# Optimization experiments

Hardware: AMD Instinct MI355X
Metric: run time of the kernel (lower is better)

The kernel has to match this reference:

```python
import jax, jax.numpy as jnp
import numpy as np

B, S, D, H = 2, 2048, 1024, 16
DH = D // H
DFF = 4 * D
EPS = 1e-5


def layer_norm(x, w, b):
    m = jnp.mean(x, axis=-1, keepdims=True)
    v = jnp.mean((x - m) ** 2, axis=-1, keepdims=True)
    return (x - m) / jnp.sqrt(v + EPS) * w + b


def setup_inputs() -> dict:
    key = jax.random.key(0)
    ks = jax.random.split(key, 12)
    s = 0.02
    x = jax.random.normal(ks[0], (B, S, D), dtype=jnp.float32)
    mask = jnp.tril(jnp.ones((S, S), dtype=jnp.int32))  # causal mask, 0 = blocked
    Wq = jax.random.normal(ks[1], (H, D, DH), dtype=jnp.float32) * s
    Wk = jax.random.normal(ks[2], (H, D, DH), dtype=jnp.float32) * s
    Wv = jax.random.normal(ks[3], (H, D, DH), dtype=jnp.float32) * s
    Wo = jax.random.normal(ks[4], (D, D), dtype=jnp.float32) * s
    bo = jnp.zeros((D,), dtype=jnp.float32)
    W1 = jax.random.normal(ks[5], (D, DFF), dtype=jnp.float32) * s
    b1 = jnp.zeros((DFF,), dtype=jnp.float32)
    W2 = jax.random.normal(ks[6], (DFF, D), dtype=jnp.float32) * s
    b2 = jnp.zeros((D,), dtype=jnp.float32)
    ln1_w = jnp.ones((D,), dtype=jnp.float32)
    ln1_b = jnp.zeros((D,), dtype=jnp.float32)
    ln2_w = jnp.ones((D,), dtype=jnp.float32)
    ln2_b = jnp.zeros((D,), dtype=jnp.float32)
    return {"x": x, "mask": mask, "Wq": Wq, "Wk": Wk, "Wv": Wv, "Wo": Wo,
            "bo": bo, "W1": W1, "b1": b1, "W2": W2, "b2": b2,
            "ln1_w": ln1_w, "ln1_b": ln1_b, "ln2_w": ln2_w, "ln2_b": ln2_b}


def reference(x, mask, Wq, Wk, Wv, Wo, bo, W1, b1, W2, b2,
              ln1_w, ln1_b, ln2_w, ln2_b):
    # --- pre-LN attention ---
    xn = layer_norm(x, ln1_w, ln1_b)
    q = jnp.einsum('bsd,hdk->bhsk', xn, Wq)  # [B,H,S,DH]
    k = jnp.einsum('bsd,hdk->bhsk', xn, Wk)
    v = jnp.einsum('bsd,hdk->bhsk', xn, Wv)
    scores = jnp.einsum('bhik,bhjk->bhij', q, k) / jnp.sqrt(jnp.float32(DH))
    scores = jnp.where(mask == 0, jnp.float32(-1e9), scores)  # mask broadcasts [S,S]->[B,H,S,S]
    attn = jax.nn.softmax(scores, axis=-1)
    o = jnp.einsum('bhij,bhjk->bhik', attn, v)        # [B,H,S,DH]
    o = o.transpose(0, 2, 1, 3).reshape(x.shape[0], x.shape[1], D)  # concat heads
    attn_out = o @ Wo + bo
    x = x + attn_out
    # --- pre-LN FFN ---
    xn2 = layer_norm(x, ln2_w, ln2_b)
    h = jax.nn.relu(xn2 @ W1 + b1)
    x = x + (h @ W2 + b2)
    return x
```

## Files before the change

### kernel.cpp

```cpp
#include <hip/hip_runtime.h>
#include <hip/hip_bf16.h>
#include <stdint.h>

#define DEV static __device__ __forceinline__

using f32x4  = __attribute__((ext_vector_type(4))) float;
using bf16x4 = __attribute__((ext_vector_type(4))) __bf16;
using bf16x8 = __attribute__((ext_vector_type(8))) __bf16;

constexpr int SEQ = 2048;

DEV unsigned short f2bf(float f) {
  union { float f; unsigned u; } c; c.f = f;
  unsigned u = c.u;
  u += 0x7fffu + ((u >> 16) & 1u);
  return (unsigned short)(u >> 16);
}

DEV float wred_sum(float v) {
  #pragma unroll
  for (int m = 32; m > 0; m >>= 1) v += __shfl_xor(v, m, 64);
  return v;
}

DEV void g2l16(const unsigned short* g, unsigned short* l) {
  __builtin_amdgcn_global_load_lds(
      (const __attribute__((address_space(1))) void*)g,
      (__attribute__((address_space(3))) void*)l, 16, 0, 0);
}

DEV int xcd_map(int bid, int nwg) {
  const int cpx = nwg >> 3;
  return (bid & 7) * cpx + (bid >> 3);
}

__global__ __launch_bounds__(256) void convw_all(
    const float* __restrict__ Wq, const float* __restrict__ Wk,
    const float* __restrict__ Wv, const float* __restrict__ Wo,
    const float* __restrict__ W1, const float* __restrict__ W2,
    unsigned short* __restrict__ WqkvT, unsigned short* __restrict__ WoT,
    unsigned short* __restrict__ W1T,   unsigned short* __restrict__ W2T)
{
  const int blk = blockIdx.x;
  const float* inh; unsigned short* outh; int K, Nh, n0, k0;
  if (blk < 768) {
    const int seg = blk >> 8, l = blk & 255;
    const int head = l >> 4, kt = l & 15;
    const float* in = seg == 0 ? Wq : seg == 1 ? Wk : Wv;
    inh  = in + (size_t)head * 1024 * 64;
    outh = WqkvT + (size_t)seg * 1024 * 1024 + (size_t)head * 64 * 1024;
    K = 1024; Nh = 64; n0 = 0; k0 = kt * 64;
  } else if (blk < 1024) {
    const int l = blk - 768; inh = Wo; outh = WoT; K = 1024; Nh = 1024;
    n0 = (l & 15) * 64; k0 = (l >> 4) * 64;
  } else if (blk < 2048) {
    const int l = blk - 1024; inh = W1; outh = W1T; K = 1024; Nh = 4096;
    n0 = (l & 63) * 64; k0 = (l >> 6) * 64;
  } else {
    const int l = blk - 2048; inh = W2; outh = W2T; K = 4096; Nh = 1024;
    n0 = (l & 15) * 64; k0 = (l >> 4) * 64;
  }
  __shared__ float t[64][65];
  const int tid = threadIdx.x;
  #pragma unroll
  for (int r = 0; r < 4; ++r) {
    const int idx = tid + 256 * r;
    const int k = idx >> 4, c = (idx & 15) * 4;
    const float4 v = *(const float4*)(inh + (size_t)(k0 + k) * Nh + n0 + c);
    t[c + 0][k] = v.x; t[c + 1][k] = v.y; t[c + 2][k] = v.z; t[c + 3][k] = v.w;
  }
  __syncthreads();
  #pragma unroll
  for (int r = 0; r < 4; ++r) {
    const int idx = tid + 256 * r;
    const int n = idx >> 4, k4 = (idx & 15) * 4;
    ushort4 o;
    o.x = f2bf(t[n][k4 + 0]); o.y = f2bf(t[n][k4 + 1]);
    o.z = f2bf(t[n][k4 + 2]); o.w = f2bf(t[n][k4 + 3]);
    *(ushort4*)(outh + (size_t)(n0 + n) * K + k0 + k4) = o;
  }
}

__global__ __launch_bounds__(256) void ln_kernel(
    const float* __restrict__ x, const float* __restrict__ w,
    const float* __restrict__ b, unsigned short* __restrict__ out)
{
  const int row = blockIdx.x;
  const int tid = threadIdx.x;
  const float4 v = ((const float4*)(x + (size_t)row * 1024))[tid];
  float s  = v.x + v.y + v.z + v.w;
  float s2 = v.x*v.x + v.y*v.y + v.z*v.z + v.w*v.w;
  s = wred_sum(s); s2 = wred_sum(s2);
  __shared__ float rs[4], rs2[4];
  const int wave = tid >> 6, lane = tid & 63;
  if (lane == 0) { rs[wave] = s; rs2[wave] = s2; }
  __syncthreads();
  const float S  = rs[0] + rs[1] + rs[2] + rs[3];
  const float S2 = rs2[0] + rs2[1] + rs2[2] + rs2[3];
  const float mean = S * (1.f / 1024.f);
  const float var  = S2 * (1.f / 1024.f) - mean * mean;
  const float inv  = rsqrtf(var + 1e-5f);
  const float4 wv = ((const float4*)w)[tid];
  const float4 bv = ((const float4*)b)[tid];
  ushort4 o;
  o.x = f2bf((v.x - mean) * inv * wv.x + bv.x);
  o.y = f2bf((v.y - mean) * inv * wv.y + bv.y);
  o.z = f2bf((v.z - mean) * inv * wv.z + bv.z);
  o.w = f2bf((v.w - mean) * inv * wv.w + bv.w);
  ((ushort4*)(out + (size_t)row * 1024))[tid] = o;
}

template<int EPI>
__global__ __launch_bounds__(256) void gemm_kp(
    const unsigned short* __restrict__ A, const unsigned short* __restrict__ BT,
    void* __restrict__ Cout, const float* __restrict__ bias,
    const float* __restrict__ res, int M, int N, int K)
{
  __shared__ unsigned short sA[3][128 * 64];
  __shared__ unsigned short sB[3][64 * 64];
  const int tid = threadIdx.x;
  const int wave = tid >> 6, lane = tid & 63;
  const int wr = wave >> 1, wc = wave & 1;
  const int bid = xcd_map(blockIdx.y * gridDim.x + blockIdx.x, gridDim.x * gridDim.y);
  const int m0 = (bid / gridDim.x) * 128, n0 = (bid % gridDim.x) * 64;
  const int lr = lane & 15, lg = lane >> 4;
  const int wb = tid & 192;

  const f32x4 zero = {0.f, 0.f, 0.f, 0.f};
  f32x4 acc[4][2];
  #pragma unroll
  for (int i = 0; i < 4; ++i)
    #pragma unroll
    for (int j = 0; j < 2; ++j) acc[i][j] = zero;

  auto STAGE = [&](int slot, int kt) {
    const int k0 = kt * 64;
    #pragma unroll
    for (int r = 0; r < 4; ++r) {
      const int c = tid + 256 * r;
      const int row = c >> 3;
      const int so = ((c & 7) ^ (row & 7)) * 8;
      g2l16(A + (size_t)(m0 + row) * K + k0 + so, sA[slot] + (size_t)(wb + 256 * r) * 8);
    }
    #pragma unroll
    for (int r = 0; r < 2; ++r) {
      const int c = tid + 256 * r;
      const int row = c >> 3;
      const int so = ((c & 7) ^ (row & 7)) * 8;
      g2l16(BT + (size_t)(n0 + row) * K + k0 + so, sB[slot] + (size_t)(wb + 256 * r) * 8);
    }
  };

  const int nt = K / 64;
  STAGE(0, 0); STAGE(1, 1);

  for (int t = 0; t < nt; ++t) {
    asm volatile("s_waitcnt vmcnt(6)" ::: "memory");
    __builtin_amdgcn_s_barrier();
    const int slot = t % 3;
    bf16x8 af[4][2], bfr[2][2];
    #pragma unroll
    for (int i = 0; i < 4; ++i) {
      const int row = wr * 64 + i * 16 + lr;
      #pragma unroll
      for (int kk = 0; kk < 2; ++kk)
        af[i][kk] = *(const bf16x8*)(sA[slot] + row * 64 + (((kk * 4 + lg) ^ (row & 7)) << 3));
    }
    #pragma unroll
    for (int j = 0; j < 2; ++j) {
      const int row = wc * 32 + j * 16 + lr;
      #pragma unroll
      for (int kk = 0; kk < 2; ++kk)
        bfr[j][kk] = *(const bf16x8*)(sB[slot] + row * 64 + (((kk * 4 + lg) ^ (row & 7)) << 3));
    }
    __builtin_amdgcn_s_setprio(1);
    #pragma unroll
    for (int i = 0; i < 4; ++i)
      #pragma unroll
      for (int j = 0; j < 2; ++j)
        #pragma unroll
        for (int kk = 0; kk < 2; ++kk)
          acc[i][j] = __builtin_amdgcn_mfma_f32_16x16x32_bf16(af[i][kk], bfr[j][kk], acc[i][j], 0, 0, 0);
    __builtin_amdgcn_s_setprio(0);
    const int nx = (t + 2 < nt) ? t + 2 : nt - 1;
    STAGE((t + 2) % 3, nx);
  }
  asm volatile("s_waitcnt vmcnt(0)" ::: "memory");

  #pragma unroll
  for (int i = 0; i < 4; ++i) {
    #pragma unroll
    for (int j = 0; j < 2; ++j) {
      #pragma unroll
      for (int r = 0; r < 4; ++r) {
        const int row = m0 + wr * 64 + i * 16 + lg * 4 + r;
        const int col = n0 + wc * 32 + j * 16 + lr;
        const float v = acc[i][j][r];
        if (EPI == 1) {
          ((float*)Cout)[(size_t)row * N + col] = v + bias[col] + res[(size_t)row * N + col];
        } else {
          ((unsigned short*)Cout)[(size_t)row * N + col] = f2bf(v);
        }
      }
    }
  }
}

template<int EPI>
__global__ __launch_bounds__(512) void gemm256(
    const unsigned short* __restrict__ A, const unsigned short* __restrict__ BT,
    void* __restrict__ Cout, const float* __restrict__ bias,
    int M, int N, int K)
{
  __shared__ unsigned short sA[2][256 * 64];
  __shared__ unsigned short sB[2][256 * 64];
  const int tid = threadIdx.x;
  const int lane = tid & 63;
  const int wave = tid >> 6;
  const int wm = wave >> 2, wn = wave & 3;
  const int bid = xcd_map(blockIdx.y * gridDim.x + blockIdx.x, gridDim.x * gridDim.y);
  const int m0 = (bid / gridDim.x) * 256, n0 = (bid % gridDim.x) * 256;
  const int lr = lane & 15, lg = lane >> 4;

  const f32x4 zero = {0.f, 0.f, 0.f, 0.f};
  f32x4 acc[8][4];
  #pragma unroll
  for (int i = 0; i < 8; ++i)
    #pragma unroll
    for (int j = 0; j < 4; ++j) acc[i][j] = zero;

  auto STAGE = [&](int buf, int k0) {
    #pragma unroll
    for (int r = 0; r < 4; ++r) {
      const int c = tid + 512 * r;
      const int row = c >> 3;
      const int slot = (c & 7) ^ (row & 7);
      const int cb = (tid & 448) + 512 * r;
      g2l16(A  + (size_t)(m0 + row) * K + k0 + slot * 8, sA[buf] + (size_t)cb * 8);
      g2l16(BT + (size_t)(n0 + row) * K + k0 + slot * 8, sB[buf] + (size_t)cb * 8);
    }
  };
  auto RD = [&](const unsigned short* base, int R, int C) -> const bf16x8* {
    return (const bf16x8*)(base + R * 64 + ((((C >> 3) ^ (R & 7))) << 3));
  };

  const int nt = K / 64;
  STAGE(0, 0);
  asm volatile("s_waitcnt vmcnt(0)" ::: "memory");
  __syncthreads();

  for (int t = 0; t < nt; ++t) {
    const int buf = t & 1;
    if (t + 1 < nt) STAGE(buf ^ 1, (t + 1) * 64);
    #pragma unroll
    for (int p = 0; p < 4; ++p) {
      const int ih = p >> 1, jh = p & 1;
      bf16x8 af[4][2], bfr[2][2];
      #pragma unroll
      for (int i = 0; i < 4; ++i)
        #pragma unroll
        for (int kk = 0; kk < 2; ++kk)
          af[i][kk] = *RD(sA[buf], wm * 128 + (ih * 4 + i) * 16 + lr, kk * 32 + lg * 8);
      #pragma unroll
      for (int j = 0; j < 2; ++j)
        #pragma unroll
        for (int kk = 0; kk < 2; ++kk)
          bfr[j][kk] = *RD(sB[buf], wn * 64 + (jh * 2 + j) * 16 + lr, kk * 32 + lg * 8);
      __builtin_amdgcn_s_setprio(1);
      #pragma unroll
      for (int i = 0; i < 4; ++i)
        #pragma unroll
        for (int j = 0; j < 2; ++j)
          #pragma unroll
          for (int kk = 0; kk < 2; ++kk)
            acc[ih * 4 + i][jh * 2 + j] = __builtin_amdgcn_mfma_f32_16x16x32_bf16(
                af[i][kk], bfr[j][kk], acc[ih * 4 + i][jh * 2 + j], 0, 0, 0);
      __builtin_amdgcn_s_setprio(0);
      if (p < 3) __builtin_amdgcn_s_barrier();
    }
    asm volatile("s_waitcnt vmcnt(0)" ::: "memory");
    __builtin_amdgcn_s_barrier();
  }

  #pragma unroll
  for (int i = 0; i < 8; ++i) {
    #pragma unroll
    for (int j = 0; j < 4; ++j) {
      #pragma unroll
      for (int r = 0; r < 4; ++r) {
        const int row = m0 + wm * 128 + i * 16 + lg * 4 + r;
        const int col = n0 + wn * 64 + j * 16 + lr;
        float v = acc[i][j][r];
        if (EPI == 0) {
          if (col < 1024) v *= 0.18033688f;
          ((unsigned short*)Cout)[(size_t)row * N + col] = f2bf(v);
        } else {
          float t2 = v + bias[col];
          t2 = t2 > 0.f ? t2 : 0.f;
          ((unsigned short*)Cout)[(size_t)row * N + col] = f2bf(t2);
        }
      }
    }
  }
}

constexpr int VPAD = 136;

__global__ __launch_bounds__(512) void attn_mfma(
    const unsigned short* __restrict__ qkv, unsigned short* __restrict__ o)
{
  const int p  = blockIdx.x >> 5;
  const int bh = blockIdx.x & 31;
  const int b = bh >> 4, h = bh & 15;
  const int tid = threadIdx.x;
  const int wave = tid >> 6, lane = tid & 63;
  const int grp = wave >> 2, wv = wave & 3;
  const int lr = lane & 15, lg = lane >> 4;

  const int qi = grp ? p : (31 - p);
  const int mynt = (qi >> 1) + 1;
  const int nt_long = ((31 - p) >> 1) + 1;
  const int q0 = qi * 64;

  __shared__ unsigned short Ks[128 * 64];
  __shared__ unsigned short Vs[64 * VPAD];
  __shared__ unsigned short Ps[8][16 * VPAD];

  const size_t qbase = ((size_t)(b * SEQ + q0 + wv * 16 + lr)) * 3072 + h * 64;
  bf16x8 qb[2];
  qb[0] = *(const bf16x8*)(qkv + qbase + lg * 8);
  qb[1] = *(const bf16x8*)(qkv + qbase + 32 + lg * 8);

  const f32x4 zero = {0.f, 0.f, 0.f, 0.f};
  f32x4 o_acc[4];
  #pragma unroll
  for (int dn = 0; dn < 4; ++dn) o_acc[dn] = zero;
  float m_run = -1e30f, l_run = 0.f;

  for (int t = 0; t < nt_long; ++t) {
    const int j0 = t * 128;
    __syncthreads();
    #pragma unroll
    for (int r = 0; r < 2; ++r) {
      const int c = tid + 512 * r;
      const int row = c >> 3;
      const int slot = (c & 7) ^ (row & 7);
      const size_t gsrc = ((size_t)(b * SEQ + j0 + row)) * 3072 + 1024 + h * 64 + slot * 8;
      g2l16(qkv + gsrc, Ks + (size_t)((tid & 448) + 512 * r) * 8);
    }
    #pragma unroll
    for (int r = 0; r < 2; ++r) {
      const int c = tid + 512 * r;
      const int key = c & 127, dseg = c >> 7;
      const size_t base = ((size_t)(b * SEQ + j0 + key)) * 3072 + 2048 + h * 64 + dseg * 8;
      int4 rv = *(const int4*)(qkv + base);
      const unsigned short* u = (const unsigned short*)&rv;
      #pragma unroll
      for (int e = 0; e < 8; ++e) Vs[(dseg * 8 + e) * VPAD + key] = u[e];
    }
    __syncthreads();

    if (t < mynt) {
      f32x4 s[8];
      __builtin_amdgcn_s_setprio(1);
      #pragma unroll
      for (int n = 0; n < 8; ++n) {
        const int row = n * 16 + lr;
        const bf16x8 kf0 = *(const bf16x8*)(Ks + row * 64 + ((lg ^ (row & 7)) << 3));
        const bf16x8 kf1 = *(const bf16x8*)(Ks + row * 64 + (((4 + lg) ^ (row & 7)) << 3));
        s[n] = __builtin_amdgcn_mfma_f32_16x16x32_bf16(kf0, qb[0], zero, 0, 0, 0);
        s[n] = __builtin_amdgcn_mfma_f32_16x16x32_bf16(kf1, qb[1], s[n], 0, 0, 0);
      }
      __builtin_amdgcn_s_setprio(0);

      const bool diag = (t == mynt - 1);
      float zm = -3e38f;
      if (diag) {
        const int q = q0 + wv * 16 + lr;
        const int kbase = j0 + lg * 4;
        #pragma unroll
        for (int n = 0; n < 8; ++n)
          #pragma unroll
          for (int r = 0; r < 4; ++r) {
            float z = s[n][r];
            if (kbase + n * 16 + r > q) z = -3e38f;
            s[n][r] = z;
            zm = fmaxf(zm, z);
          }
      } else {
        #pragma unroll
        for (int n = 0; n < 8; ++n)
          zm = fmaxf(fmaxf(fmaxf(zm, s[n][0]), fmaxf(s[n][1], s[n][2])), s[n][3]);
      }
      zm = fmaxf(zm, __shfl_xor(zm, 16, 64));
      zm = fmaxf(zm, __shfl_xor(zm, 32, 64));

      const bool skip = __all(zm - m_run <= 10.f);
      if (!skip) {
        const float mnew = fmaxf(m_run, zm);
        const float alpha = exp2f(m_run - mnew);
        m_run = mnew;
        l_run *= alpha;
        float a4[4];
        #pragma unroll
        for (int r = 0; r < 4; ++r) a4[r] = __shfl(alpha, lg * 4 + r, 64);
        #pragma unroll
        for (int dn = 0; dn < 4; ++dn)
          #pragma unroll
          for (int r = 0; r < 4; ++r) o_acc[dn][r] *= a4[r];
      }

      float psum = 0.f;
      #pragma unroll
      for (int n = 0; n < 8; ++n) {
        float p0 = exp2f(s[n][0] - m_run); psum += p0;
        float p1 = exp2f(s[n][1] - m_run); psum += p1;
        float p2 = exp2f(s[n][2] - m_run); psum += p2;
        float p3 = exp2f(s[n][3] - m_run); psum += p3;
        bf16x4 pw = { (__bf16)p0, (__bf16)p1, (__bf16)p2, (__bf16)p3 };
        *(bf16x4*)(&Ps[wave][lr * VPAD + n * 16 + lg * 4]) = pw;
      }
      psum += __shfl_xor(psum, 16, 64);
      psum += __shfl_xor(psum, 32, 64);
      l_run += psum;

      bf16x8 pa[4];
      #pragma unroll
      for (int kk = 0; kk < 4; ++kk)
        pa[kk] = *(const bf16x8*)(&Ps[wave][lr * VPAD + kk * 32 + lg * 8]);
      __builtin_amdgcn_s_setprio(1);
      #pragma unroll
      for (int dn = 0; dn < 4; ++dn) {
        #pragma unroll
        for (int kk = 0; kk < 4; ++kk) {
          const bf16x8 vf = *(const bf16x8*)(Vs + (dn * 16 + lr) * VPAD + kk * 32 + lg * 8);
          o_acc[dn] = __builtin_amdgcn_mfma_f32_16x16x32_bf16(pa[kk], vf, o_acc[dn], 0, 0, 0);
        }
      }
      __builtin_amdgcn_s_setprio(0);
    }
  }

  float linv[4];
  #pragma unroll
  for (int r = 0; r < 4; ++r) linv[r] = 1.f / __shfl(l_run, lg * 4 + r, 64);
  #pragma unroll
  for (int r = 0; r < 4; ++r) {
    const int qq = q0 + wv * 16 + lg * 4 + r;
    const size_t obase = ((size_t)(b * SEQ + qq)) * 1024 + h * 64;
    #pragma unroll
    for (int dn = 0; dn < 4; ++dn)
      o[obase + dn * 16 + lr] = f2bf(o_acc[dn][r] * linv[r]);
  }
}

extern "C" void kernel_launch(void* const* d_in, const int* in_sizes, int n_in,
                              void* d_out, int out_size, void* d_ws, size_t ws_size,
                              hipStream_t stream) {
  const float* x    = (const float*)d_in[0];
  const float* Wq   = (const float*)d_in[2];
  const float* Wk   = (const float*)d_in[3];
  const float* Wv   = (const float*)d_in[4];
  const float* Wo   = (const float*)d_in[5];
  const float* bo   = (const float*)d_in[6];
  const float* W1   = (const float*)d_in[7];
  const float* b1   = (const float*)d_in[8];
  const float* W2   = (const float*)d_in[9];
  const float* b2   = (const float*)d_in[10];
  const float* ln1w = (const float*)d_in[11];
  const float* ln1b = (const float*)d_in[12];
  const float* ln2w = (const float*)d_in[13];
  const float* ln2b = (const float*)d_in[14];

  char* ws = (char*)d_ws;
  unsigned short* WqkvT = (unsigned short*)(ws);
  unsigned short* WoT   = (unsigned short*)(ws + 6291456);
  unsigned short* W1T   = (unsigned short*)(ws + 8388608);
  unsigned short* W2T   = (unsigned short*)(ws + 16777216);
  unsigned short* xn    = (unsigned short*)(ws + 25165824);
  float*          x1    = (float*)        (ws + 33554432);
  unsigned short* qkv   = (unsigned short*)(ws + 50331648);
  unsigned short* oc    = (unsigned short*)(ws + 75497472);
  unsigned short* hbuf  = qkv;

  convw_all<<<3072, 256, 0, stream>>>(Wq, Wk, Wv, Wo, W1, W2, WqkvT, WoT, W1T, W2T);
  ln_kernel<<<4096, 256, 0, stream>>>(x, ln1w, ln1b, xn);
  gemm256<0><<<dim3(12, 16), 512, 0, stream>>>(xn, WqkvT, qkv, nullptr, 4096, 3072, 1024);
  attn_mfma<<<512, 512, 0, stream>>>(qkv, oc);
  gemm_kp<1><<<dim3(16, 32), 256, 0, stream>>>(oc, WoT, x1, bo, x, 4096, 1024, 1024);
  ln_kernel<<<4096, 256, 0, stream>>>(x1, ln2w, ln2b, xn);
  gemm256<2><<<dim3(16, 16), 512, 0, stream>>>(xn, W1T, hbuf, b1, 4096, 4096, 1024);
  gemm_kp<1><<<dim3(16, 32), 256, 0, stream>>>(hbuf, W2T, (float*)d_out, b2, x1, 4096, 1024, 4096);
}
```

Measured before the change: 223.3 us.

## Restructure 256x256 GEMM into triple-buffered K=32 pipeline with one barrier per step

The 256x256 bf16 GEMM used for QKV and FFN1 now works in K-steps of 32 with a three-slot LDS ring instead of two slots of K=64. Loads are issued two steps ahead and waited on with vmcnt(4). This removes the intra-tile barriers and the full vmcnt(0) drain that the old loop had every iteration. LDS use drops from 128KB to 96KB, but each K-step does fewer MFMAs per barrier, and the tail issues redundant loads of the last tile.

```diff
diff --git a/kernel.cpp b/kernel.cpp
--- a/kernel.cpp
+++ b/kernel.cpp
@@ -207,20 +207,20 @@
 }
 
 template<int EPI>
-__global__ __launch_bounds__(512) void gemm256(
+__global__ __launch_bounds__(512) void gemm256v2(
     const unsigned short* __restrict__ A, const unsigned short* __restrict__ BT,
     void* __restrict__ Cout, const float* __restrict__ bias,
     int M, int N, int K)
 {
-  __shared__ unsigned short sA[2][256 * 64];
-  __shared__ unsigned short sB[2][256 * 64];
+  __shared__ unsigned short sA[3][256 * 32];
+  __shared__ unsigned short sB[3][256 * 32];
   const int tid = threadIdx.x;
-  const int lane = tid & 63;
-  const int wave = tid >> 6;
+  const int wave = tid >> 6, lane = tid & 63;
   const int wm = wave >> 2, wn = wave & 3;
   const int bid = xcd_map(blockIdx.y * gridDim.x + blockIdx.x, gridDim.x * gridDim.y);
   const int m0 = (bid / gridDim.x) * 256, n0 = (bid % gridDim.x) * 256;
   const int lr = lane & 15, lg = lane >> 4;
+  const int wb = tid & 448;
 
   const f32x4 zero = {0.f, 0.f, 0.f, 0.f};
   f32x4 acc[8][4];
@@ -229,58 +229,48 @@
     #pragma unroll
     for (int j = 0; j < 4; ++j) acc[i][j] = zero;
 
-  auto STAGE = [&](int buf, int k0) {
-    #pragma unroll
-    for (int r = 0; r < 4; ++r) {
+  auto STAGE = [&](int slot, int kt) {
+    const int k0 = kt * 32;
+    #pragma unroll
+    for (int r = 0; r < 2; ++r) {
       const int c = tid + 512 * r;
-      const int row = c >> 3;
-      const int slot = (c & 7) ^ (row & 7);
-      const int cb = (tid & 448) + 512 * r;
-      g2l16(A  + (size_t)(m0 + row) * K + k0 + slot * 8, sA[buf] + (size_t)cb * 8);
-      g2l16(BT + (size_t)(n0 + row) * K + k0 + slot * 8, sB[buf] + (size_t)cb * 8);
+      const int row = c >> 2;
+      const int so = ((c & 3) ^ (row & 3)) * 8;
+      const int cb = wb + 512 * r;
+      g2l16(A  + (size_t)(m0 + row) * K + k0 + so, sA[slot] + (size_t)cb * 8);
+      g2l16(BT + (size_t)(n0 + row) * K + k0 + so, sB[slot] + (size_t)cb * 8);
     }
   };
-  auto RD = [&](const unsigned short* base, int R, int C) -> const bf16x8* {
-    return (const bf16x8*)(base + R * 64 + ((((C >> 3) ^ (R & 7))) << 3));
-  };
-
-  const int nt = K / 64;
-  STAGE(0, 0);
+
+  const int nt = K / 32;
+  STAGE(0, 0); STAGE(1, 1);
+
+  for (int t = 0; t < nt; ++t) {
+    asm volatile("s_waitcnt vmcnt(4)" ::: "memory");
+    __builtin_amdgcn_s_barrier();
+    const int slot = t % 3;
+    bf16x8 af[8], bfr[4];
+    #pragma unroll
+    for (int i = 0; i < 8; ++i) {
+      const int row = wm * 128 + i * 16 + lr;
+      af[i] = *(const bf16x8*)(sA[slot] + row * 32 + ((lg ^ (row & 3)) << 3));
+    }
+    #pragma unroll
+    for (int j = 0; j < 4; ++j) {
+      const int row = wn * 64 + j * 16 + lr;
+      bfr[j] = *(const bf16x8*)(sB[slot] + row * 32 + ((lg ^ (row & 3)) << 3));
+    }
+    __builtin_amdgcn_s_setprio(1);
+    #pragma unroll
+    for (int i = 0; i < 8; ++i)
+      #pragma unroll
+      for (int j = 0; j < 4; ++j)
+        acc[i][j] = __builtin_amdgcn_mfma_f32_16x16x32_bf16(af[i], bfr[j], acc[i][j], 0, 0, 0);
+    __builtin_amdgcn_s_setprio(0);
+    const int nx = (t + 2 < nt) ? t + 2 : nt - 1;
+    STAGE((t + 2) % 3, nx);
+  }
   asm volatile("s_waitcnt vmcnt(0)" ::: "memory");
-  __syncthreads();
-
-  for (int t = 0; t < nt; ++t) {
-    const int buf = t & 1;
-    if (t + 1 < nt) STAGE(buf ^ 1, (t + 1) * 64);
-    #pragma unroll
-    for (int p = 0; p < 4; ++p) {
-      const int ih = p >> 1, jh = p & 1;
-      bf16x8 af[4][2], bfr[2][2];
-      #pragma unroll
-      for (int i = 0; i < 4; ++i)
-        #pragma unroll
-        for (int kk = 0; kk < 2; ++kk)
-          af[i][kk] = *RD(sA[buf], wm * 128 + (ih * 4 + i) * 16 + lr, kk * 32 + lg * 8);
-      #pragma unroll
-      for (int j = 0; j < 2; ++j)
-        #pragma unroll
-        for (int kk = 0; kk < 2; ++kk)
-          bfr[j][kk] = *RD(sB[buf], wn * 64 + (jh * 2 + j) * 16 + lr, kk * 32 + lg * 8);
-      __builtin_amdgcn_s_setprio(1);
-      #pragma unroll
-      for (int i = 0; i < 4; ++i)
-        #pragma unroll
-        for (int j = 0; j < 2; ++j)
-          #pragma unroll
-          for (int kk = 0; kk < 2; ++kk)
-            acc[ih * 4 + i][jh * 2 + j] = __builtin_amdgcn_mfma_f32_16x16x32_bf16(
-                af[i][kk], bfr[j][kk], acc[ih * 4 + i][jh * 2 + j], 0, 0, 0);
-      __builtin_amdgcn_s_setprio(0);
-      if (p < 3) __builtin_amdgcn_s_barrier();
-    }
-    asm volatile("s_waitcnt vmcnt(0)" ::: "memory");
-    __builtin_amdgcn_s_barrier();
-  }
 
   #pragma unroll
   for (int i = 0; i < 8; ++i) {
@@ -485,10 +475,10 @@
 
   convw_all<<<3072, 256, 0, stream>>>(Wq, Wk, Wv, Wo, W1, W2, WqkvT, WoT, W1T, W2T);
   ln_kernel<<<4096, 256, 0, stream>>>(x, ln1w, ln1b, xn);
-  gemm256<0><<<dim3(12, 16), 512, 0, stream>>>(xn, WqkvT, qkv, nullptr, 4096, 3072, 1024);
+  gemm256v2<0><<<dim3(12, 16), 512, 0, stream>>>(xn, WqkvT, qkv, nullptr, 4096, 3072, 1024);
   attn_mfma<<<512, 512, 0, stream>>>(qkv, oc);
   gemm_kp<1><<<dim3(16, 32), 256, 0, stream>>>(oc, WoT, x1, bo, x, 4096, 1024, 1024);
   ln_kernel<<<4096, 256, 0, stream>>>(x1, ln2w, ln2b, xn);
-  gemm256<2><<<dim3(16, 16), 512, 0, stream>>>(xn, W1T, hbuf, b1, 4096, 4096, 1024);
+  gemm256v2<2><<<dim3(16, 16), 512, 0, stream>>>(xn, W1T, hbuf, b1, 4096, 4096, 1024);
   gemm_kp<1><<<dim3(16, 32), 256, 0, stream>>>(hbuf, W2T, (float*)d_out, b2, x1, 4096, 1024, 4096);
 }
```

Result: no change. 221.1 us (-1.0%).
